# Performance work log

Measured on AMD Instinct MI355X. Metric: run time of the kernel, lower is better.

## Reference

```python
import jax, jax.numpy as jnp
import numpy as np

LEAKY_SLOPE = 0.2  # PyG GATv2Conv default negative_slope


def gatv2_layer(x, src, dst, Wl, Wr, att, bias, concat):
    """PyG GATv2Conv (eval mode, dropout off, self-loops already in src/dst).
    x: [N, Din]; Wl/Wr: [Din, H*C]; att: [H, C]; bias: [H*C] or [C].
    """
    N = x.shape[0]
    H, C = att.shape
    xl = (x @ Wl).reshape(N, H, C)   # source transform
    xr = (x @ Wr).reshape(N, H, C)   # target transform
    # per-edge GATv2 score: att . leakyrelu(x_l[j] + x_r[i])
    e = jax.nn.leaky_relu(xl[src] + xr[dst], negative_slope=LEAKY_SLOPE)  # [E, H, C]
    score = jnp.einsum('ehc,hc->eh', e, att)                              # [E, H]
    # segment softmax over incoming edges of each dst node
    m = jax.ops.segment_max(score, dst, num_segments=N)                   # [N, H]
    a = jnp.exp(score - m[dst])
    denom = jax.ops.segment_sum(a, dst, num_segments=N)                   # [N, H]
    alpha = a / denom[dst]                                                # [E, H]
    out = jax.ops.segment_sum(xl[src] * alpha[..., None], dst, num_segments=N)  # [N, H, C]
    out = out.reshape(N, H * C) if concat else out.mean(axis=1)
    return out + bias


def setup_inputs() -> dict:
    key = jax.random.key(0)
    ks = jax.random.split(key, 10)
    N, D, E = 20000, 128, 320000
    HID, HEADS, OUT = 64, 8, 32
    x = jax.random.normal(ks[0], (N, D), dtype=jnp.float32)
    edge_index = jax.random.randint(ks[1], (2, E), 0, N)
    glorot = lambda k, shape, fan: jax.random.normal(k, shape, jnp.float32) * (1.0 / np.sqrt(fan))
    W1l = glorot(ks[2], (D, HEADS * HID), D)
    W1r = glorot(ks[3], (D, HEADS * HID), D)
    att1 = glorot(ks[4], (HEADS, HID), HID)
    b1 = jnp.zeros((HEADS * HID,), jnp.float32)
    W2l = glorot(ks[5], (HEADS * HID, 64), HEADS * HID)
    W2r = glorot(ks[6], (HEADS * HID, 64), HEADS * HID)
    att2 = glorot(ks[7], (1, 64), 64)
    b2 = jnp.zeros((64,), jnp.float32)
    Wlin = glorot(ks[8], (64, OUT), 64)
    blin = jnp.zeros((OUT,), jnp.float32)
    return {"x": x, "edge_index": edge_index, "W1l": W1l, "W1r": W1r, "att1": att1,
            "b1": b1, "W2l": W2l, "W2r": W2r, "att2": att2, "b2": b2,
            "Wlin": Wlin, "blin": blin}


def reference(x, edge_index, W1l, W1r, att1, b1, W2l, W2r, att2, b2, Wlin, blin):
    N = x.shape[0]
    loop = jnp.arange(N)
    src = jnp.concatenate([edge_index[0], loop])  # PyG add_self_loops=True
    dst = jnp.concatenate([edge_index[1], loop])
    h = jax.nn.elu(gatv2_layer(x, src, dst, W1l, W1r, att1, b1, concat=True))
    h = jax.nn.elu(gatv2_layer(h, src, dst, W2l, W2r, att2, b2, concat=False))
    return jax.nn.elu(h @ Wlin + blin)
```

## Files before the change

kernel.cpp:

```cpp
#include <hip/hip_runtime.h>
#include <hip/hip_bf16.h>

typedef __attribute__((ext_vector_type(8))) short short8;
typedef __attribute__((ext_vector_type(4))) short short4v;
typedef __attribute__((ext_vector_type(4))) float floatx4;
typedef __attribute__((ext_vector_type(2))) float float2v;
typedef __attribute__((ext_vector_type(4))) int int4v;
typedef __attribute__((ext_vector_type(2))) int int2v;

#define LOG2E 1.44269504f

__device__ __forceinline__ short f2b(float f) {
    __hip_bfloat16 hb = __float2bfloat16(f);
    unsigned short us; __builtin_memcpy(&us, &hb, 2);
    return (short)us;
}
__device__ __forceinline__ float2v bpair(int p) {
    unsigned ulo = ((unsigned)p) << 16;
    unsigned uhi = ((unsigned)p) & 0xFFFF0000u;
    float flo, fhi;
    __builtin_memcpy(&flo, &ulo, 4);
    __builtin_memcpy(&fhi, &uhi, 4);
    float2v r; r.x = flo; r.y = fhi; return r;
}

__device__ __forceinline__ float2v pk_add(float2v a, float2v b) {
    float2v d;
    asm("v_pk_add_f32 %0, %1, %2" : "=v"(d) : "v"(a), "v"(b));
    return d;
}
__device__ __forceinline__ float2v pk_fma(float2v a, float2v b, float2v c) {
    float2v d;
    asm("v_pk_fma_f32 %0, %1, %2, %3" : "=v"(d) : "v"(a), "v"(b), "v"(c));
    return d;
}
__device__ __forceinline__ float2v pk_abs(float2v a) {
    float2v d;
    d.x = __builtin_fabsf(a.x);
    d.y = __builtin_fabsf(a.y);
    return d;
}

template<int CTRL>
__device__ __forceinline__ float dppadd(float x) {
    int xi; __builtin_memcpy(&xi, &x, 4);
    int yi = __builtin_amdgcn_update_dpp(0, xi, CTRL, 0xF, 0xF, false);
    float y; __builtin_memcpy(&y, &yi, 4);
    return x + y;
}
__device__ __forceinline__ float red8(float x) {
    x = dppadd<0xB1>(x);
    x = dppadd<0x4E>(x);
    x = dppadd<0x141>(x);
    return x;
}
__device__ __forceinline__ float red16(float x) {
    return dppadd<0x140>(red8(x));
}

__global__ void prep_all(const float* __restrict__ x,
                         const float* __restrict__ W1l, const float* __restrict__ W1r,
                         const float* __restrict__ W2l, const float* __restrict__ W2r,
                         short* __restrict__ xb, short* __restrict__ w1t,
                         short* __restrict__ w2t, int nx4,
                         const int* __restrict__ esrc, const int* __restrict__ edst,
                         int E, int N, int* __restrict__ counts,
                         unsigned short* __restrict__ srcs) {
    int tid = blockIdx.x * blockDim.x + threadIdx.x;
    int ET = E + N;
    if (tid < ET) {
        int d, s;
        if (tid < E) { d = edst[tid]; s = esrc[tid]; }
        else { d = tid - E; s = d; }
        int pos = atomicAdd(&counts[d], 1);
        if (pos < 64) srcs[(d << 6) + pos] = (unsigned short)s;
    }
    int idx = tid;
    if (idx < nx4) {
        floatx4 v = *(const floatx4*)(x + idx * 4);
        short4v o; o[0] = f2b(v[0]); o[1] = f2b(v[1]); o[2] = f2b(v[2]); o[3] = f2b(v[3]);
        *(short4v*)(xb + idx * 4) = o;
        return;
    }
    idx -= nx4;
    if (idx < 131072) {
        int n = idx >> 7, k = idx & 127;
        float v = (n < 512) ? W1l[k * 512 + n] : W1r[k * 512 + (n - 512)];
        w1t[idx] = f2b(v);
        return;
    }
    idx -= 131072;
    if (idx < 65536) {
        int n = idx >> 9, k = idx & 511;
        float v = (n < 64) ? W2l[k * 64 + n] : W2r[k * 64 + (n - 64)];
        w2t[idx] = f2b(v);
    }
}

__global__ __launch_bounds__(256) void gemm1(const short* __restrict__ A,
                                             const short* __restrict__ Bt,
                                             short* __restrict__ xl1, short* __restrict__ xr1,
                                             int M) {
    __shared__ short As[64 * 136];
    __shared__ short Bs[128 * 136];
    int t = threadIdx.x;
    int w = t >> 6, L = t & 63, q = L >> 4, s = L & 15;
    int p = blockIdx.x + (blockIdx.y << 3);
    int my = gridDim.y;
    int ww = (p & 7) * my + (p >> 3);
    int M0 = (ww >> 3) * 64, N0 = (ww & 7) * 128;
    #pragma unroll
    for (int i = 0; i < 4; ++i) {
        int c = t + i * 256;
        int r = c >> 4, col = (c & 15) * 8;
        int gr = M0 + r;
        short8 v = {};
        if (gr < M) v = *(const short8*)(A + (size_t)gr * 128 + col);
        *(short8*)(&As[r * 136 + col]) = v;
    }
    #pragma unroll
    for (int i = 0; i < 8; ++i) {
        int c = t + i * 256;
        int r = c >> 4, col = (c & 15) * 8;
        short8 v = *(const short8*)(Bt + (size_t)(N0 + r) * 128 + col);
        *(short8*)(&Bs[r * 136 + col]) = v;
    }
    __syncthreads();
    short8 a[4];
    #pragma unroll
    for (int kk = 0; kk < 4; ++kk)
        a[kk] = *(const short8*)(&As[(w * 16 + s) * 136 + kk * 32 + q * 8]);
    floatx4 acc[8] = {};
    #pragma unroll
    for (int tt = 0; tt < 8; ++tt) {
        #pragma unroll
        for (int kk = 0; kk < 4; ++kk) {
            short8 b = *(const short8*)(&Bs[(tt * 16 + s) * 136 + kk * 32 + q * 8]);
            acc[tt] = __builtin_amdgcn_mfma_f32_16x16x32_bf16(a[kk], b, acc[tt], 0, 0, 0);
        }
    }
    __syncthreads();
    #pragma unroll
    for (int tt = 0; tt < 8; ++tt) {
        #pragma unroll
        for (int rg = 0; rg < 4; ++rg) {
            int rl = w * 16 + q * 4 + rg;
            As[rl * 136 + tt * 16 + s] = f2b(acc[tt][rg]);
        }
    }
    __syncthreads();
    short* Cb = (N0 < 512) ? xl1 : xr1;
    int cb = (N0 < 512) ? N0 : N0 - 512;
    size_t M64 = (size_t)M * 64;
    #pragma unroll
    for (int i = 0; i < 4; ++i) {
        int c = t + i * 256;
        int r = c >> 4, col = (c & 15) * 8;
        int row = M0 + r;
        if (row < M) {
            short8 v = *(const short8*)(&As[r * 136 + col]);
            int cc = cb + col;
            *(short8*)(Cb + (size_t)(cc >> 6) * M64 + (size_t)row * 64 + (cc & 63)) = v;
        }
    }
}

__global__ __launch_bounds__(256) void gemm2(const short* __restrict__ A,
                                             const short* __restrict__ Bt,
                                             short* __restrict__ C, int M) {
    __shared__ short As[32 * 72];
    __shared__ short Bs[64 * 72];
    int t = threadIdx.x;
    int w = t >> 6, L = t & 63, q = L >> 4, s = L & 15;
    int rw = (w >> 1) * 16, cw = (w & 1) * 32;
    int p = blockIdx.x + gridDim.x * blockIdx.y;
    int nwg = gridDim.x * 2;
    int qq = nwg >> 3, rr = nwg & 7;
    int kx = p & 7, tx = p >> 3;
    int ww = (kx < rr ? kx * (qq + 1) : rr * (qq + 1) + (kx - rr) * qq) + tx;
    int M0 = (ww >> 1) * 32, N0 = (ww & 1) * 64;
    size_t M64 = (size_t)M * 64;
    floatx4 acc[2] = {};
    for (int k0 = 0; k0 < 512; k0 += 64) {
        {
            int r = t >> 3, col = (t & 7) * 8;
            int gr = M0 + r;
            short8 v = {};
            if (gr < M) v = *(const short8*)(A + (size_t)(k0 >> 6) * M64 + (size_t)gr * 64 + col);
            *(short8*)(&As[r * 72 + col]) = v;
        }
        #pragma unroll
        for (int i = 0; i < 2; ++i) {
            int c = t + i * 256;
            int r = c >> 3, col = (c & 7) * 8;
            short8 v = *(const short8*)(Bt + (size_t)(N0 + r) * 512 + k0 + col);
            *(short8*)(&Bs[r * 72 + col]) = v;
        }
        __syncthreads();
        #pragma unroll
        for (int kk = 0; kk < 2; ++kk) {
            short8 a = *(const short8*)(&As[(rw + s) * 72 + kk * 32 + q * 8]);
            #pragma unroll
            for (int tt = 0; tt < 2; ++tt) {
                short8 b = *(const short8*)(&Bs[(cw + tt * 16 + s) * 72 + kk * 32 + q * 8]);
                acc[tt] = __builtin_amdgcn_mfma_f32_16x16x32_bf16(a, b, acc[tt], 0, 0, 0);
            }
        }
        __syncthreads();
    }
    #pragma unroll
    for (int tt = 0; tt < 2; ++tt) {
        #pragma unroll
        for (int rg = 0; rg < 4; ++rg) {
            int rl = rw + q * 4 + rg;
            As[rl * 72 + cw + tt * 16 + s] = f2b(acc[tt][rg]);
        }
    }
    __syncthreads();
    {
        int r = t >> 3, col = (t & 7) * 8;
        int row = M0 + r;
        if (row < M) {
            short8 v = *(const short8*)(&As[r * 72 + col]);
            *(short8*)(C + (size_t)row * 128 + N0 + col) = v;
        }
    }
}

__global__ __launch_bounds__(256) void gat_l1(const short* __restrict__ xlh,
                       const short* __restrict__ xrh,
                       const int* __restrict__ counts,
                       const unsigned short* __restrict__ srcs,
                       const float* __restrict__ att, const float* __restrict__ bias,
                       short* __restrict__ h1h, int Nn) {
    int bid = blockIdx.x;
    int h = bid & 7, nb = bid >> 3;
    int t = threadIdx.x;
    int w = t >> 6, L = t & 63;
    int u = L >> 3;
    int c = L & 7;
    int o8 = c * 8;
    int i = (nb * 4 + w) * 8 + u;
    bool inode = i < Nn;
    int ic = inode ? i : 0;
    size_t slice = (size_t)h * ((size_t)Nn * 64);
    const char* Bp = (const char*)(xlh + slice);
    int co = c << 4;

    float2v xrv[4], at6[4], at4[4];
    {
        float av[8];
        *(floatx4*)av       = *(const floatx4*)(att + h * 64 + o8);
        *(floatx4*)(av + 4) = *(const floatx4*)(att + h * 64 + o8 + 4);
        int4v x4 = *(const int4v*)(xrh + slice + (size_t)ic * 64 + o8);
        #pragma unroll
        for (int k = 0; k < 4; ++k) {
            xrv[k] = bpair(x4[k]);
            at6[k].x = av[2 * k]     * (0.6f * LOG2E);
            at6[k].y = av[2 * k + 1] * (0.6f * LOG2E);
            at4[k].x = av[2 * k]     * (0.4f * LOG2E);
            at4[k].y = av[2 * k + 1] * (0.4f * LOG2E);
        }
    }
    int deg = counts[ic]; deg = deg > 64 ? 64 : deg;
    if (!inode) deg = 0;
    int degw = deg;
    degw = max(degw, __shfl_xor(degw, 8, 64));
    degw = max(degw, __shfl_xor(degw, 16, 64));
    degw = max(degw, __shfl_xor(degw, 32, 64));

    const unsigned short* sp = srcs + ((size_t)ic << 6);
    int4v J = *(const int4v*)(sp + c * 8);
    int ubase = L & 56;

    float2v acc[4] = {};
    float dnm = 0.f;

    for (int ow = 0; ow < 8; ++ow) {
        int s0 = ow << 3;
        if (s0 >= degw) break;
        int lane = ubase + ow;
        int j01 = __shfl(J[0], lane, 64);
        int j23 = __shfl(J[1], lane, 64);
        int j45 = __shfl(J[2], lane, 64);
        int j67 = __shfl(J[3], lane, 64);
        int js[8];
        js[0] = j01 & 0x7FFF; js[1] = (j01 >> 16) & 0x7FFF;
        js[2] = j23 & 0x7FFF; js[3] = (j23 >> 16) & 0x7FFF;
        js[4] = j45 & 0x7FFF; js[5] = (j45 >> 16) & 0x7FFF;
        js[6] = j67 & 0x7FFF; js[7] = (j67 >> 16) & 0x7FFF;
        int4v rows[8];
        #pragma unroll
        for (int k = 0; k < 8; ++k)
            rows[k] = *(const int4v*)(Bp + (((unsigned)js[k] << 7) + co));
        #pragma unroll
        for (int k = 0; k < 8; ++k) {
            float2v v[4]; float2v pp = {};
            #pragma unroll
            for (int q = 0; q < 4; ++q) {
                v[q] = bpair(rows[k][q]);
                float2v tv = pk_add(v[q], xrv[q]);
                pp = pk_fma(at6[q], tv, pp);
                pp = pk_fma(at4[q], pk_abs(tv), pp);
            }
            float e2 = __builtin_amdgcn_exp2f(red8(pp.x + pp.y));
            e2 = (s0 + k < deg) ? e2 : 0.f;
            dnm += e2;
            float2v ev; ev.x = e2; ev.y = e2;
            #pragma unroll
            for (int q = 0; q < 4; ++q)
                acc[q] = pk_fma(ev, v[q], acc[q]);
        }
    }

    if (inode) {
        float inv = 1.f / dnm;
        float bv[8];
        *(floatx4*)bv       = *(const floatx4*)(bias + h * 64 + o8);
        *(floatx4*)(bv + 4) = *(const floatx4*)(bias + h * 64 + o8 + 4);
        short8 ov;
        #pragma unroll
        for (int k = 0; k < 4; ++k) {
            float ox = fmaf(acc[k].x, inv, bv[2 * k]);
            float oy = fmaf(acc[k].y, inv, bv[2 * k + 1]);
            ox = ox > 0.f ? ox : __expf(ox) - 1.f;
            oy = oy > 0.f ? oy : __expf(oy) - 1.f;
            ov[2 * k] = f2b(ox);
            ov[2 * k + 1] = f2b(oy);
        }
        *(short8*)(h1h + slice + (size_t)i * 64 + o8) = ov;
    }
}

__global__ __launch_bounds__(256) void gat_l2_fin(const short* __restrict__ x2,
                        const int* __restrict__ counts,
                        const unsigned short* __restrict__ srcs,
                        const float* __restrict__ att, const float* __restrict__ bias,
                        const float* __restrict__ Wlin, const float* __restrict__ blin,
                        float* __restrict__ out, int Nn) {
    __shared__ float Ws[2048];
    __shared__ float bs[32];
    __shared__ float h2s[4][64];
    int t = threadIdx.x;
    for (int idx = t; idx < 2048; idx += 256) Ws[idx] = Wlin[idx];
    if (t < 32) bs[t] = blin[t];
    __syncthreads();
    int w = t >> 6, L = t & 63;
    int i = blockIdx.x * 4 + w;
    if (i >= Nn) return;
    int g = L >> 4;
    int lc = L & 15;
    int c4 = lc * 4;
    float2v xrv[2], at6[2], at4[2];
    {
        int2v xv = *(const int2v*)(x2 + (i << 7) + 64 + c4);
        xrv[0] = bpair(xv.x);
        xrv[1] = bpair(xv.y);
        floatx4 a4 = *(const floatx4*)(att + c4);
        at6[0].x = a4[0] * (0.6f * LOG2E); at6[0].y = a4[1] * (0.6f * LOG2E);
        at6[1].x = a4[2] * (0.6f * LOG2E); at6[1].y = a4[3] * (0.6f * LOG2E);
        at4[0].x = a4[0] * (0.4f * LOG2E); at4[0].y = a4[1] * (0.4f * LOG2E);
        at4[1].x = a4[2] * (0.4f * LOG2E); at4[1].y = a4[3] * (0.4f * LOG2E);
    }
    float dnm = 0.f;
    float2v acc0 = {}, acc1 = {};
    int kb = i << 6;
    int deg = counts[i]; deg = deg > 64 ? 64 : deg;
    int ke = kb + deg;
    const int2v* x2i = (const int2v*)x2;

    auto doedge = [&](int2v Vv, bool val) {
        float2v v0 = bpair(Vv.x), v1 = bpair(Vv.y);
        float2v t0 = pk_add(v0, xrv[0]), t1 = pk_add(v1, xrv[1]);
        float2v pp = pk_fma(at6[0], t0, at4[0] * pk_abs(t0));
        pp = pk_fma(at6[1], t1, pp);
        pp = pk_fma(at4[1], pk_abs(t1), pp);
        float e = val ? __builtin_amdgcn_exp2f(red16(pp.x + pp.y)) : 0.f;
        dnm += e;
        float2v e2; e2.x = e; e2.y = e;
        acc0 = pk_fma(e2, v0, acc0);
        acc1 = pk_fma(e2, v1, acc1);
    };

    for (int k0 = kb; k0 < ke; k0 += 16) {
        int ka = k0 + g, kc = k0 + 4 + g, kd = k0 + 8 + g, kf = k0 + 12 + g;
        bool va = ka < ke, vb = kc < ke, vc = kd < ke, vd = kf < ke;
        int ja = srcs[va ? ka : kb];
        int jb = srcs[vb ? kc : kb];
        int jc = srcs[vc ? kd : kb];
        int jd = srcs[vd ? kf : kb];
        int2v Va = x2i[(ja << 5) + lc];
        int2v Vb = x2i[(jb << 5) + lc];
        int2v Vc = x2i[(jc << 5) + lc];
        int2v Vd = x2i[(jd << 5) + lc];
        doedge(Va, va);
        doedge(Vb, vb);
        doedge(Vc, vc);
        doedge(Vd, vd);
    }
    #pragma unroll
    for (int m = 16; m <= 32; m <<= 1) {
        dnm += __shfl_xor(dnm, m, 64);
        acc0.x += __shfl_xor(acc0.x, m, 64);
        acc0.y += __shfl_xor(acc0.y, m, 64);
        acc1.x += __shfl_xor(acc1.x, m, 64);
        acc1.y += __shfl_xor(acc1.y, m, 64);
    }
    float inv = 1.f / dnm;
    floatx4 bv = *(const floatx4*)(bias + c4);
    float o0 = fmaf(acc0.x, inv, bv[0]);
    float o1 = fmaf(acc0.y, inv, bv[1]);
    float o2 = fmaf(acc1.x, inv, bv[2]);
    float o3 = fmaf(acc1.y, inv, bv[3]);
    o0 = o0 > 0.f ? o0 : __expf(o0) - 1.f;
    o1 = o1 > 0.f ? o1 : __expf(o1) - 1.f;
    o2 = o2 > 0.f ? o2 : __expf(o2) - 1.f;
    o3 = o3 > 0.f ? o3 : __expf(o3) - 1.f;
    if (L < 16) {
        floatx4 hv; hv[0] = o0; hv[1] = o1; hv[2] = o2; hv[3] = o3;
        *(floatx4*)(&h2s[w][c4]) = hv;
    }
    int oc = L & 31;
    float accl = 0.f;
    #pragma unroll
    for (int kk = 0; kk < 16; ++kk) {
        floatx4 hvv = *(const floatx4*)(&h2s[w][kk * 4]);
        accl = fmaf(hvv[0], Ws[(kk * 4 + 0) * 32 + oc], accl);
        accl = fmaf(hvv[1], Ws[(kk * 4 + 1) * 32 + oc], accl);
        accl = fmaf(hvv[2], Ws[(kk * 4 + 2) * 32 + oc], accl);
        accl = fmaf(hvv[3], Ws[(kk * 4 + 3) * 32 + oc], accl);
    }
    if (L < 32) {
        float r = accl + bs[oc];
        r = r > 0.f ? r : __expf(r) - 1.f;
        out[(size_t)i * 32 + oc] = r;
    }
}

extern "C" void kernel_launch(void* const* d_in, const int* in_sizes, int n_in,
                              void* d_out, int out_size, void* d_ws, size_t ws_size,
                              hipStream_t stream) {
    const float* x    = (const float*)d_in[0];
    const int*   ei   = (const int*)d_in[1];
    const float* W1l  = (const float*)d_in[2];
    const float* W1r  = (const float*)d_in[3];
    const float* att1 = (const float*)d_in[4];
    const float* b1   = (const float*)d_in[5];
    const float* W2l  = (const float*)d_in[6];
    const float* W2r  = (const float*)d_in[7];
    const float* att2 = (const float*)d_in[8];
    const float* b2   = (const float*)d_in[9];
    const float* Wlin = (const float*)d_in[10];
    const float* blin = (const float*)d_in[11];

    const int N  = in_sizes[0] / 128;
    const int E  = in_sizes[1] / 2;

    char* w = (char*)d_ws;
    size_t cur = 0;
    auto take = [&](size_t bytes) -> void* {
        void* p = w + cur;
        cur = (cur + bytes + 255) & ~(size_t)255;
        return p;
    };
    int*            counts = (int*)take((size_t)N * 4);
    unsigned short* srcs   = (unsigned short*)take((size_t)N * 64 * 2);
    short* xb     = (short*)take((size_t)N * 128 * 2);
    short* w1t    = (short*)take((size_t)1024 * 128 * 2);
    short* w2t    = (short*)take((size_t)128 * 512 * 2);
    short* xl1    = (short*)take((size_t)N * 512 * 2);
    short* xr1    = (short*)take((size_t)N * 512 * 2);
    short* h1     = (short*)take((size_t)N * 512 * 2);
    short* x2     = (short*)take((size_t)N * 128 * 2);

    hipMemsetAsync(counts, 0, (size_t)N * 4, stream);
    int nx4 = N * 32;
    int nconv = nx4 + 131072 + 65536;
    int nprep = (E + N) > nconv ? (E + N) : nconv;
    prep_all<<<(nprep + 255) / 256, 256, 0, stream>>>(x, W1l, W1r, W2l, W2r, xb, w1t, w2t,
                                                      nx4, ei, ei + E, E, N, counts, srcs);

    gemm1<<<dim3(8, (N + 63) / 64), 256, 0, stream>>>(xb, w1t, xl1, xr1, N);
    gat_l1<<<8 * ((N + 31) / 32), 256, 0, stream>>>(xl1, xr1, counts, srcs, att1, b1, h1, N);

    gemm2<<<dim3((N + 31) / 32, 2), 256, 0, stream>>>(h1, w2t, x2, N);
    gat_l2_fin<<<(N + 3) / 4, 256, 0, stream>>>(x2, counts, srcs, att2, b2, Wlin, blin,
                                                (float*)d_out, N);
}
```

Measured before the change: 197.2 us.

## Double-buffer neighbor row gathers in layer-1 GAT aggregation kernel

```diff
diff --git a/kernel.cpp b/kernel.cpp
--- a/kernel.cpp
+++ b/kernel.cpp
@@ -240,12 +240,14 @@
     int u = L >> 3;
     int c = L & 7;
     int o8 = c * 8;
-    int i = (nb * 4 + w) * 8 + u;
+    int wbase = (nb * 4 + w) * 8;
+    if (wbase >= Nn) return;
+    int i = wbase + u;
     bool inode = i < Nn;
     int ic = inode ? i : 0;
     size_t slice = (size_t)h * ((size_t)Nn * 64);
-    const char* Bp = (const char*)(xlh + slice);
-    int co = c << 4;
+    const char* Bh = (const char*)(xlh + slice);
+    unsigned co = (unsigned)(c << 4);
 
     float2v xrv[4], at6[4], at4[4];
     {
@@ -270,29 +272,14 @@
     degw = max(degw, __shfl_xor(degw, 32, 64));
 
     const unsigned short* sp = srcs + ((size_t)ic << 6);
-    int4v J = *(const int4v*)(sp + c * 8);
-    int ubase = L & 56;
 
     float2v acc[4] = {};
     float dnm = 0.f;
 
-    for (int ow = 0; ow < 8; ++ow) {
-        int s0 = ow << 3;
-        if (s0 >= degw) break;
-        int lane = ubase + ow;
-        int j01 = __shfl(J[0], lane, 64);
-        int j23 = __shfl(J[1], lane, 64);
-        int j45 = __shfl(J[2], lane, 64);
-        int j67 = __shfl(J[3], lane, 64);
-        int js[8];
-        js[0] = j01 & 0x7FFF; js[1] = (j01 >> 16) & 0x7FFF;
-        js[2] = j23 & 0x7FFF; js[3] = (j23 >> 16) & 0x7FFF;
-        js[4] = j45 & 0x7FFF; js[5] = (j45 >> 16) & 0x7FFF;
-        js[6] = j67 & 0x7FFF; js[7] = (j67 >> 16) & 0x7FFF;
-        int4v rows[8];
-        #pragma unroll
-        for (int k = 0; k < 8; ++k)
-            rows[k] = *(const int4v*)(Bp + (((unsigned)js[k] << 7) + co));
+    auto ldrow = [&](unsigned j) -> int4v {
+        return *(const int4v*)(Bh + ((j << 7) + co));
+    };
+    auto mathblk = [&](const int4v* rows, int s0) {
         #pragma unroll
         for (int k = 0; k < 8; ++k) {
             float2v v[4]; float2v pp = {};
@@ -311,6 +298,37 @@
             for (int q = 0; q < 4; ++q)
                 acc[q] = pk_fma(ev, v[q], acc[q]);
         }
+    };
+
+    int nblk = (degw + 7) >> 3;
+    unsigned short jA[8], jB[8];
+    int4v rA[8], rB[8];
+    #pragma unroll
+    for (int k = 0; k < 8; ++k) jA[k] = sp[k];
+    #pragma unroll
+    for (int k = 0; k < 8; ++k) rA[k] = ldrow(jA[k]);
+    #pragma unroll
+    for (int k = 0; k < 8; ++k) jB[k] = sp[8 + k];
+    int b = 0;
+    for (;;) {
+        if (b + 1 < nblk) {
+            #pragma unroll
+            for (int k = 0; k < 8; ++k) rB[k] = ldrow(jB[k]);
+            int nbase = (b + 2) * 8;
+            #pragma unroll
+            for (int k = 0; k < 8; ++k) jA[k] = sp[nbase + k];
+        }
+        mathblk(rA, b * 8);
+        if (++b >= nblk) break;
+        if (b + 1 < nblk) {
+            #pragma unroll
+            for (int k = 0; k < 8; ++k) rA[k] = ldrow(jA[k]);
+            int nbase = (b + 2) * 8;
+            #pragma unroll
+            for (int k = 0; k < 8; ++k) jB[k] = sp[nbase + k];
+        }
+        mathblk(rB, b * 8);
+        if (++b >= nblk) break;
     }
 
     if (inode) {
```

New measurement: 198.3 us. No clear change (+0.6%).

## Sort layer-1 nodes by in-degree and fuse x bf16 conversion into gemm1

Applied to the files above, without the earlier changes.

```diff
diff --git a/kernel.cpp b/kernel.cpp
--- a/kernel.cpp
+++ b/kernel.cpp
@@ -58,11 +58,9 @@
     return dppadd<0x140>(red8(x));
 }
 
-__global__ void prep_all(const float* __restrict__ x,
-                         const float* __restrict__ W1l, const float* __restrict__ W1r,
+__global__ void prep_all(const float* __restrict__ W1l, const float* __restrict__ W1r,
                          const float* __restrict__ W2l, const float* __restrict__ W2r,
-                         short* __restrict__ xb, short* __restrict__ w1t,
-                         short* __restrict__ w2t, int nx4,
+                         short* __restrict__ w1t, short* __restrict__ w2t,
                          const int* __restrict__ esrc, const int* __restrict__ edst,
                          int E, int N, int* __restrict__ counts,
                          unsigned short* __restrict__ srcs) {
@@ -76,13 +74,6 @@
         if (pos < 64) srcs[(d << 6) + pos] = (unsigned short)s;
     }
     int idx = tid;
-    if (idx < nx4) {
-        floatx4 v = *(const floatx4*)(x + idx * 4);
-        short4v o; o[0] = f2b(v[0]); o[1] = f2b(v[1]); o[2] = f2b(v[2]); o[3] = f2b(v[3]);
-        *(short4v*)(xb + idx * 4) = o;
-        return;
-    }
-    idx -= nx4;
     if (idx < 131072) {
         int n = idx >> 7, k = idx & 127;
         float v = (n < 512) ? W1l[k * 512 + n] : W1r[k * 512 + (n - 512)];
@@ -97,7 +88,28 @@
     }
 }
 
-__global__ __launch_bounds__(256) void gemm1(const short* __restrict__ A,
+__global__ void bin_count(const int* __restrict__ counts, int* __restrict__ bincnt,
+                          int N) {
+    int i = blockIdx.x * blockDim.x + threadIdx.x;
+    if (i < N) { int d = counts[i]; d = d > 64 ? 64 : d; atomicAdd(&bincnt[d], 1); }
+}
+__global__ void bin_prefix(const int* __restrict__ bincnt, int* __restrict__ binoff) {
+    if (threadIdx.x == 0) {
+        int s = 0;
+        for (int b = 0; b <= 64; ++b) { binoff[b] = s; s += bincnt[b]; }
+    }
+}
+__global__ void bin_scatter(const int* __restrict__ counts, int* __restrict__ binoff,
+                            int* __restrict__ perm, int N) {
+    int i = blockIdx.x * blockDim.x + threadIdx.x;
+    if (i < N) {
+        int d = counts[i]; d = d > 64 ? 64 : d;
+        int p = atomicAdd(&binoff[d], 1);
+        perm[p] = i;
+    }
+}
+
+__global__ __launch_bounds__(256) void gemm1(const float* __restrict__ A,
                                              const short* __restrict__ Bt,
                                              short* __restrict__ xl1, short* __restrict__ xr1,
                                              int M) {
@@ -110,13 +122,14 @@
     int ww = (p & 7) * my + (p >> 3);
     int M0 = (ww >> 3) * 64, N0 = (ww & 7) * 128;
     #pragma unroll
-    for (int i = 0; i < 4; ++i) {
+    for (int i = 0; i < 8; ++i) {
         int c = t + i * 256;
-        int r = c >> 4, col = (c & 15) * 8;
+        int r = c >> 5, col4 = c & 31;
         int gr = M0 + r;
-        short8 v = {};
-        if (gr < M) v = *(const short8*)(A + (size_t)gr * 128 + col);
-        *(short8*)(&As[r * 136 + col]) = v;
+        floatx4 v = {};
+        if (gr < M) v = *(const floatx4*)(A + (size_t)gr * 128 + col4 * 4);
+        short4v o; o[0] = f2b(v[0]); o[1] = f2b(v[1]); o[2] = f2b(v[2]); o[3] = f2b(v[3]);
+        *(short4v*)(&As[r * 136 + col4 * 4]) = o;
     }
     #pragma unroll
     for (int i = 0; i < 8; ++i) {
@@ -231,6 +244,7 @@
                        const short* __restrict__ xrh,
                        const int* __restrict__ counts,
                        const unsigned short* __restrict__ srcs,
+                       const int* __restrict__ perm,
                        const float* __restrict__ att, const float* __restrict__ bias,
                        short* __restrict__ h1h, int Nn) {
     int bid = blockIdx.x;
@@ -240,9 +254,9 @@
     int u = L >> 3;
     int c = L & 7;
     int o8 = c * 8;
-    int i = (nb * 4 + w) * 8 + u;
-    bool inode = i < Nn;
-    int ic = inode ? i : 0;
+    int idx = (nb * 4 + w) * 8 + u;
+    bool inode = idx < Nn;
+    int ic = perm[inode ? idx : 0];
     size_t slice = (size_t)h * ((size_t)Nn * 64);
     const char* Bp = (const char*)(xlh + slice);
     int co = c << 4;
@@ -328,7 +342,7 @@
             ov[2 * k] = f2b(ox);
             ov[2 * k + 1] = f2b(oy);
         }
-        *(short8*)(h1h + slice + (size_t)i * 64 + o8) = ov;
+        *(short8*)(h1h + slice + (size_t)ic * 64 + o8) = ov;
     }
 }
 
@@ -465,7 +479,9 @@
     };
     int*            counts = (int*)take((size_t)N * 4);
     unsigned short* srcs   = (unsigned short*)take((size_t)N * 64 * 2);
-    short* xb     = (short*)take((size_t)N * 128 * 2);
+    int*   bincnt = (int*)take(65 * 4);
+    int*   binoff = (int*)take(65 * 4);
+    int*   perm   = (int*)take((size_t)N * 4);
     short* w1t    = (short*)take((size_t)1024 * 128 * 2);
     short* w2t    = (short*)take((size_t)128 * 512 * 2);
     short* xl1    = (short*)take((size_t)N * 512 * 2);
@@ -474,14 +490,18 @@
     short* x2     = (short*)take((size_t)N * 128 * 2);
 
     hipMemsetAsync(counts, 0, (size_t)N * 4, stream);
-    int nx4 = N * 32;
-    int nconv = nx4 + 131072 + 65536;
-    int nprep = (E + N) > nconv ? (E + N) : nconv;
-    prep_all<<<(nprep + 255) / 256, 256, 0, stream>>>(x, W1l, W1r, W2l, W2r, xb, w1t, w2t,
-                                                      nx4, ei, ei + E, E, N, counts, srcs);
-
-    gemm1<<<dim3(8, (N + 63) / 64), 256, 0, stream>>>(xb, w1t, xl1, xr1, N);
-    gat_l1<<<8 * ((N + 31) / 32), 256, 0, stream>>>(xl1, xr1, counts, srcs, att1, b1, h1, N);
+    hipMemsetAsync(bincnt, 0, 65 * 4, stream);
+    int nprep = (E + N) > 196608 ? (E + N) : 196608;
+    prep_all<<<(nprep + 255) / 256, 256, 0, stream>>>(W1l, W1r, W2l, W2r, w1t, w2t,
+                                                      ei, ei + E, E, N, counts, srcs);
+
+    bin_count<<<(N + 255) / 256, 256, 0, stream>>>(counts, bincnt, N);
+    bin_prefix<<<1, 64, 0, stream>>>(bincnt, binoff);
+    bin_scatter<<<(N + 255) / 256, 256, 0, stream>>>(counts, binoff, perm, N);
+
+    gemm1<<<dim3(8, (N + 63) / 64), 256, 0, stream>>>(x, w1t, xl1, xr1, N);
+    gat_l1<<<8 * ((N + 31) / 32), 256, 0, stream>>>(xl1, xr1, counts, srcs, perm,
+                                                    att1, b1, h1, N);
 
     gemm2<<<dim3((N + 31) / 32, 2), 256, 0, stream>>>(h1, w2t, x2, N);
     gat_l2_fin<<<(N + 3) / 4, 256, 0, stream>>>(x2, counts, srcs, att2, b2, Wlin, blin,
```

Measured after the change: 308.0 us. 56.1% more time.
